# Performance work log

Hardware: AMD Instinct MI355X
Metric: run time of the kernel (lower is better)

## Reference

```python
import jax, jax.numpy as jnp
import numpy as np

B, IN_SEQ, HID_SEQ, OUT_SEQ = 2, 2048, 2048, 2048
C_IN, C_OUT, H = 1024, 1024, 16
HD = C_OUT // H  # 64


def _linear_params(key, out_f, in_f):
    kw, kb = jax.random.split(key)
    bound = 1.0 / np.sqrt(in_f)
    w = jax.random.uniform(kw, (out_f, in_f), jnp.float32, -bound, bound)
    b = jax.random.uniform(kb, (out_f,), jnp.float32, -bound, bound)
    return w, b


def setup_inputs() -> dict:
    key = jax.random.key(0)
    ks = jax.random.split(key, 6)
    x = jax.random.normal(ks[0], (B, IN_SEQ, C_IN), jnp.float32)
    w_hseq, b_hseq = _linear_params(ks[1], HID_SEQ, IN_SEQ)
    wq, bq = _linear_params(ks[2], C_OUT, C_IN)
    wk, bk = _linear_params(ks[3], C_OUT, C_IN)
    wv, bv = _linear_params(ks[4], C_OUT, C_IN)
    w_oseq, b_oseq = _linear_params(ks[5], OUT_SEQ, HID_SEQ)
    return {"x": x, "w_hseq": w_hseq, "b_hseq": b_hseq,
            "wq": wq, "bq": bq, "wk": wk, "bk": bk, "wv": wv, "bv": bv,
            "w_oseq": w_oseq, "b_oseq": b_oseq}


def reference(x, w_hseq, b_hseq, wq, bq, wk, bk, wv, bv, w_oseq, b_oseq):
    b = x.shape[0]
    # seq-axis projection: Linear(in_seq -> hidden_seq) applied to x.transpose(1,2)
    # xh[b, t, c] = sum_s x[b, s, c] * w_hseq[t, s] + b_hseq[t]
    xh = jnp.einsum('bsc,ts->btc', x, w_hseq) + b_hseq[:, None]
    q = (xh @ wq.T + bq).reshape(b, HID_SEQ, H, HD).transpose(0, 2, 1, 3)  # [B,H,Sh,hd]
    k = (xh @ wk.T + bk).reshape(b, HID_SEQ, H, HD).transpose(0, 2, 1, 3)
    v = (xh @ wv.T + bv).reshape(b, HID_SEQ, H, HD).transpose(0, 2, 1, 3)
    scores = jnp.einsum('bhqd,bhkd->bhqk', q, k) / np.sqrt(HD).astype(np.float32)
    attn = jax.nn.softmax(scores, axis=-1)                       # [B,H,Sh,Sh]
    flex = jnp.einsum('bhqk,ok->bhqo', attn, w_oseq) + b_oseq    # [B,H,Sh,So]
    # flexscale.transpose(-2,-1) @ v contracts over the QUERY axis q
    out = jnp.einsum('bhqo,bhqd->bhod', flex, v)                 # [B,H,So,hd]
    return out.transpose(0, 2, 1, 3).reshape(b, OUT_SEQ, C_OUT)
```

## Files before the change

kernel.cpp:

```cpp
#include <hip/hip_runtime.h>
#include <hip/hip_bf16.h>

typedef unsigned short u16;
typedef unsigned int u32;
typedef unsigned long long u64;
typedef __attribute__((ext_vector_type(8))) short s16x8;
typedef __attribute__((ext_vector_type(4))) float f32x4;
typedef __attribute__((ext_vector_type(16))) float f32x16;

#define SCL 0.1803368867f

#if __has_builtin(__builtin_amdgcn_exp2f)
#define EXP2(x) __builtin_amdgcn_exp2f(x)
#else
#define EXP2(x) exp2f(x)
#endif

__device__ __forceinline__ float bf2f(u16 v){ u32 u = ((u32)v)<<16; return __builtin_bit_cast(float,u); }
__device__ __forceinline__ u16 f2bf(float f){
  u32 u = __builtin_bit_cast(u32,f);
  u += 0x7fff + ((u>>16)&1);
  return (u16)(u>>16);
}
__device__ __forceinline__ u32 pkbf(float a, float b){
  u32 ua = __builtin_bit_cast(u32,a) + 0x8000u;
  u32 ub = __builtin_bit_cast(u32,b) + 0x8000u;
  return (ua>>16) | (ub & 0xFFFF0000u);
}
__device__ __forceinline__ void glds16(const u16* g, const u16* lds_u){
  __builtin_amdgcn_global_load_lds(
      (const __attribute__((address_space(1))) void*)(u64)g,
      (__attribute__((address_space(3))) void*)(u32)(u64)lds_u,
      16, 0, 0);
}
__device__ __forceinline__ f32x4 mfma16(s16x8 a, s16x8 b, f32x4 c){
  return __builtin_amdgcn_mfma_f32_16x16x32_bf16(a,b,c,0,0,0);
}
__device__ __forceinline__ f32x16 mfma32(s16x8 a, s16x8 b, f32x16 c){
  return __builtin_amdgcn_mfma_f32_32x32x16_bf16(a,b,c,0,0,0);
}

__global__ __launch_bounds__(256) void detect_dtype(const u16* __restrict__ x, u32* __restrict__ flag){
  __shared__ int cnt;
  if (threadIdx.x==0) cnt = 0;
  __syncthreads();
  int local = 0;
  for (int i = threadIdx.x; i < 4096; i += 256){
    u16 v = x[2*i];
    int e = (v>>7)&0xFF;
    if (e >= 140 || e <= 100) local++;
  }
  atomicAdd(&cnt, local);
  __syncthreads();
  if (threadIdx.x==0) *flag = (cnt > 1024) ? 1u : 0u;
}

struct CvtArgs { const void* src[10]; u16* dst[10]; int n[10]; };

__global__ __launch_bounds__(256) void convert_inputs(CvtArgs a, const u32* __restrict__ flag){
  const int which = blockIdx.y;
  const int n = a.n[which];
  const int base = blockIdx.x*2048 + threadIdx.x;
  if (base >= n) return;
  u16* dst = a.dst[which];
  if (*flag){
    const float* s = (const float*)a.src[which];
    #pragma unroll
    for (int j=0;j<8;j++){ int i = base + j*256; if (i<n) dst[i] = f2bf(s[i]); }
  } else {
    const u16* s = (const u16*)a.src[which];
    #pragma unroll
    for (int j=0;j<8;j++){ int i = base + j*256; if (i<n) dst[i] = s[i]; }
  }
}

__global__ __launch_bounds__(256) void transpose_x(
    const void* __restrict__ src, const u32* __restrict__ flag, u16* __restrict__ dst)
{
  __shared__ u16 T[64][72];
  const int s0 = blockIdx.x*64, c0 = blockIdx.y*64, b = blockIdx.z;
  const int t = threadIdx.x;
  const int r = t>>2, cc = (t&3)*16;
  const long off = ((long)(b*2048 + s0 + r))*1024 + c0 + cc;
  if (*flag){
    const float* p = (const float*)src + off;
    #pragma unroll
    for (int j=0;j<16;j++) T[r][cc+j] = f2bf(p[j]);
  } else {
    const u16* p = (const u16*)src + off;
    *(s16x8*)&T[r][cc]   = *(const s16x8*)p;
    *(s16x8*)&T[r][cc+8] = *(const s16x8*)(p+8);
  }
  __syncthreads();
  {
    const int orow = t&63, oc = (t>>6)*16;
    u16 tmp[16];
    #pragma unroll
    for (int j=0;j<16;j++) tmp[j] = T[oc+j][orow];
    u16* q = dst + (long)b*2097152 + (long)(c0+orow)*2048 + s0 + oc;
    *(s16x8*)q     = *(s16x8*)&tmp[0];
    *(s16x8*)(q+8) = *(s16x8*)&tmp[8];
  }
}

__global__ __launch_bounds__(256) void rowsum_part(const u16* __restrict__ qkv, float* __restrict__ svp){
  const int c = blockIdx.x*256 + threadIdx.x;
  const int b = c>>10, cc = c&1023;
  const int tz = blockIdx.y;
  const u16* p = qkv + ((long)(b*2048 + tz*256))*3072 + 2048 + cc;
  float s = 0.f;
  #pragma unroll 8
  for (int i=0;i<256;i++) s += bf2f(p[(long)i*3072]);
  svp[tz*2048 + c] = s;
}
__global__ __launch_bounds__(256) void rowsum_fin(const float* __restrict__ svp, float* __restrict__ sv){
  const int c = blockIdx.x*256 + threadIdx.x;
  float s = 0.f;
  #pragma unroll
  for (int z=0;z<8;z++) s += svp[z*2048 + c];
  sv[c] = s;
}

template<int BN, int BMODE, bool DYN, bool QS>
__global__ __launch_bounds__(256) void gemm_t(
    const u16* __restrict__ A, const u16* __restrict__ B,
    const u16* __restrict__ bias, const float* __restrict__ r1col,
    const u32* __restrict__ dflag, void* __restrict__ C,
    int K, int lda, int ldb, int ldc,
    long aBatch, long bBatch, long cBatch)
{
  constexpr int BM = 128;
  constexpr int ACH = BM/64, BCH = BN/64;
  constexpr int MI = (BN==128) ? 4 : 2;
  __shared__ u16 As[2][BM*32];
  __shared__ u16 Bs[2][BN*32];
  const int t = threadIdx.x, w = t>>6, quad = (t&63)>>4, l16 = t&15;
  const int z = blockIdx.z;
  const int m0 = blockIdx.x*BM, n0 = blockIdx.y*BN;
  const u16* Ag = A + (long)z*aBatch + (long)m0*lda;
  const u16* Bg = B + (long)z*bBatch + (long)n0*ldb;
  const int wm = (BN==128) ? (w>>1)*64 : w*32;
  const int wn = (BN==128) ? (w&1)*64 : 0;

  auto stage = [&](int buf, int k0){
    #pragma unroll
    for (int i=0;i<ACH;i++){
      const int chunk = i*256 + t;
      glds16(Ag + (long)(chunk>>2)*lda + k0 + (chunk&3)*8, &As[buf][(i*256 + w*64)*8]);
    }
    #pragma unroll
    for (int i=0;i<BCH;i++){
      const int chunk = i*256 + t;
      glds16(Bg + (long)(chunk>>2)*ldb + k0 + (chunk&3)*8, &Bs[buf][(i*256 + w*64)*8]);
    }
  };

  f32x4 acc[MI][4];
  #pragma unroll
  for (int i=0;i<MI;i++)
    #pragma unroll
    for (int j=0;j<4;j++) acc[i][j] = (f32x4){0.f,0.f,0.f,0.f};

  stage(0, 0);
  const int nk = K>>5;
  for (int kt=0; kt<nk; ++kt){
    __syncthreads();
    if (kt+1 < nk) stage((kt+1)&1, (kt+1)<<5);
    const u16* as = As[kt&1];
    const u16* bs = Bs[kt&1];
    s16x8 a[MI], bb[4];
    #pragma unroll
    for (int i=0;i<MI;i++) a[i] = *(const s16x8*)&as[(wm + i*16 + l16)*32 + quad*8];
    #pragma unroll
    for (int j=0;j<4;j++)  bb[j]= *(const s16x8*)&bs[(wn + j*16 + l16)*32 + quad*8];
    #pragma unroll
    for (int i=0;i<MI;i++)
      #pragma unroll
      for (int j=0;j<4;j++)
        acc[i][j] = mfma16(a[i], bb[j], acc[i][j]);
  }

  bool f32o = false;
  if (DYN) f32o = (*dflag != 0);
  #pragma unroll
  for (int i=0;i<MI;i++){
    #pragma unroll
    for (int j=0;j<4;j++){
      const int col = n0 + wn + j*16 + l16;
      #pragma unroll
      for (int r=0;r<4;r++){
        const int row = m0 + wm + i*16 + quad*4 + r;
        float vv = acc[i][j][r];
        if (BMODE==1) vv += bf2f(bias[row]);
        if (BMODE==2) vv += bf2f(bias[col]);
        if (BMODE==3) vv += bf2f(bias[row]) * r1col[z*1024 + col];
        if (QS){ if (col < 1024) vv *= SCL; }
        const long idx = (long)z*cBatch + (long)row*ldc + col;
        if (DYN && f32o) ((float*)C)[idx] = vv;
        else             ((u16*)C)[idx]   = f2bf(vv);
      }
    }
  }
}

__global__ __launch_bounds__(256) void attn_stats(const u16* __restrict__ qkv, u16* __restrict__ VtG){
  __shared__ u16 Qs[64][68];
  __shared__ u16 Ks[64][68];
  __shared__ float red[2][64];
  __shared__ float ilv[64];
  const int q0 = blockIdx.x*64, bh = blockIdx.y, b = bh>>4, h = bh&15;
  const int t = threadIdx.x, w = t>>6, l32 = t&31, half = (t&63)>>5;
  const int wq = w>>1, wk = w&1;
  {
    const int r = t>>2, cc = (t&3)*16;
    const u16* p = &qkv[((long)(b*2048 + q0 + r))*3072 + h*64 + cc];
    *(s16x8*)&Qs[r][cc]   = *(const s16x8*)p;
    *(s16x8*)&Qs[r][cc+8] = *(const s16x8*)(p+8);
  }
  __syncthreads();
  s16x8 aq[4];
  #pragma unroll
  for (int u=0;u<4;u++) aq[u] = *(s16x8*)&Qs[wq*32 + l32][u*16 + half*8];
  float lp[16];
  #pragma unroll
  for (int r=0;r<16;r++) lp[r] = 0.f;

  for (int kc=0; kc<2048; kc+=64){
    __syncthreads();
    {
      const int r = t>>2, cc = (t&3)*16;
      const u16* p = &qkv[((long)(b*2048 + kc + r))*3072 + 1024 + h*64 + cc];
      *(s16x8*)&Ks[r][cc]   = *(const s16x8*)p;
      *(s16x8*)&Ks[r][cc+8] = *(const s16x8*)(p+8);
    }
    __syncthreads();
    s16x8 kb[4];
    #pragma unroll
    for (int u=0;u<4;u++) kb[u] = *(s16x8*)&Ks[wk*32 + l32][u*16 + half*8];
    f32x16 acc = {};
    #pragma unroll
    for (int u=0;u<4;u++) acc = mfma32(aq[u], kb[u], acc);
    #pragma unroll
    for (int r=0;r<16;r++) lp[r] += EXP2(acc[r]);
  }
  #pragma unroll
  for (int off=1; off<32; off<<=1)
    #pragma unroll
    for (int r=0;r<16;r++) lp[r] += __shfl_xor(lp[r], off);
  if (l32 == 0){
    #pragma unroll
    for (int r=0;r<16;r++)
      red[wk][wq*32 + 4*half + (r&3) + 8*(r>>2)] = lp[r];
  }
  __syncthreads();
  if (t < 64) ilv[t] = 1.f / (red[0][t] + red[1][t]);
  __syncthreads();
  {
    const int r = t>>2, cc = (t&3)*16;
    const u16* p = &qkv[((long)(b*2048 + q0 + r))*3072 + 2048 + h*64 + cc];
    const float sc = ilv[r];
    s16x8 v0 = *(const s16x8*)p, v1 = *(const s16x8*)(p+8);
    #pragma unroll
    for (int j=0;j<8;j++){
      Qs[r][cc+j]   = f2bf(bf2f((u16)v0[j])*sc);
      Qs[r][cc+8+j] = f2bf(bf2f((u16)v1[j])*sc);
    }
  }
  __syncthreads();
  {
    const int orow = t&63, oc = (t>>6)*16;
    u16 tmp[16];
    #pragma unroll
    for (int j=0;j<16;j++) tmp[j] = Qs[oc+j][orow];
    u16* q = VtG + (long)b*2097152 + (long)(h*64+orow)*2048 + q0 + oc;
    *(s16x8*)q     = *(s16x8*)&tmp[0];
    *(s16x8*)(q+8) = *(s16x8*)&tmp[8];
  }
}

__global__ __launch_bounds__(256) void attn_pv(
    const u16* __restrict__ qkv, const u16* __restrict__ VtG, u16* __restrict__ Mt)
{
  __shared__ u16 KPs[64][68];
  __shared__ u16 Qs[64][68];
  __shared__ u16 Vs[64][68];
  const int k0 = blockIdx.x*64, bh = blockIdx.y, b = bh>>4, h = bh&15;
  const int t = threadIdx.x, w = t>>6, l32 = t&31, half = (t&63)>>5;
  const int wr = w>>1, wk = w&1;
  const int sr = t>>2, scc = (t&3)*16;
  {
    const u16* p = &qkv[((long)(b*2048 + k0 + sr))*3072 + 1024 + h*64 + scc];
    *(s16x8*)&KPs[sr][scc]   = *(const s16x8*)p;
    *(s16x8*)&KPs[sr][scc+8] = *(const s16x8*)(p+8);
  }
  __syncthreads();
  s16x8 kb[4];
  #pragma unroll
  for (int u=0;u<4;u++) kb[u] = *(s16x8*)&KPs[wk*32 + l32][u*16 + half*8];

  f32x16 accM = {};
  for (int q0=0; q0<2048; q0+=64){
    __syncthreads();
    {
      const u16* pq = &qkv[((long)(b*2048 + q0 + sr))*3072 + h*64 + scc];
      *(s16x8*)&Qs[sr][scc]   = *(const s16x8*)pq;
      *(s16x8*)&Qs[sr][scc+8] = *(const s16x8*)(pq+8);
      const u16* pv = &VtG[((long)(b*1024 + h*64 + sr))*2048 + q0 + scc];
      *(s16x8*)&Vs[sr][scc]   = *(const s16x8*)pv;
      *(s16x8*)&Vs[sr][scc+8] = *(const s16x8*)(pv+8);
    }
    __syncthreads();
    s16x8 aq[4];
    #pragma unroll
    for (int u=0;u<4;u++) aq[u] = *(s16x8*)&Qs[wr*32 + l32][u*16 + half*8];
    f32x16 acc = {};
    #pragma unroll
    for (int u=0;u<4;u++) acc = mfma32(aq[u], kb[u], acc);
    const int kcol = wk*32 + l32;
    #pragma unroll
    for (int g=0; g<4; g++){
      float p0 = EXP2(acc[4*g+0]);
      float p1 = EXP2(acc[4*g+1]);
      float p2 = EXP2(acc[4*g+2]);
      float p3 = EXP2(acc[4*g+3]);
      u64 v = (u64)pkbf(p0,p1) | ((u64)pkbf(p2,p3) << 32);
      *(u64*)&KPs[kcol][wr*32 + 8*g + 4*half] = v;
    }
    __syncthreads();
    s16x8 av[4], bp[4];
    #pragma unroll
    for (int u=0;u<4;u++) av[u] = *(s16x8*)&Vs[wr*32 + l32][u*16 + half*8];
    #pragma unroll
    for (int u=0;u<4;u++) bp[u] = *(s16x8*)&KPs[wk*32 + l32][u*16 + half*8];
    #pragma unroll
    for (int u=0;u<4;u++) accM = mfma32(av[u], bp[u], accM);
  }
  #pragma unroll
  for (int r=0;r<16;r++){
    const int d = wr*32 + 4*half + (r&3) + 8*(r>>2);
    const int k = k0 + wk*32 + l32;
    Mt[((long)(b*1024 + h*64 + d))*2048 + k] = f2bf(accM[r]);
  }
}

extern "C" void kernel_launch(void* const* d_in, const int* in_sizes, int n_in,
                              void* d_out, int out_size, void* d_ws, size_t ws_size,
                              hipStream_t stream)
{
  (void)n_in; (void)out_size; (void)ws_size;
  char* ws = (char*)d_ws;
  u32*  dflag = (u32*)ws;            ws += 64;
  u16*  whc   = (u16*)ws;            ws += (size_t)8388608;
  u16*  wqkvc = (u16*)ws;            ws += (size_t)6291456;
  u16*  woc   = (u16*)ws;            ws += (size_t)8388608;
  u16*  bhc   = (u16*)ws;            ws += 4096;
  u16*  bqkvc = (u16*)ws;            ws += 8192;
  u16*  boc   = (u16*)ws;            ws += 4096;
  u16*  xT    = (u16*)ws;            ws += (size_t)8388608;
  u16*  xh    = (u16*)ws;            ws += (size_t)8388608;
  u16*  qkvb  = (u16*)ws;            ws += (size_t)25165824;
  u16*  VtG   = (u16*)ws;            ws += (size_t)8388608;
  u16*  Mt    = (u16*)ws;            ws += (size_t)8388608;
  float* svp  = (float*)ws;          ws += (size_t)65536;
  float* sv   = (float*)ws;          ws += 8192;

  detect_dtype<<<1,256,0,stream>>>((const u16*)d_in[0], dflag);
  CvtArgs ca;
  const void* srcs[10] = {d_in[1], d_in[2], d_in[3], d_in[4], d_in[5],
                          d_in[6], d_in[7], d_in[8], d_in[9], d_in[10]};
  u16* dsts[10] = {whc, bhc, wqkvc, bqkvc, wqkvc+1048576, bqkvc+1024,
                   wqkvc+2097152, bqkvc+2048, woc, boc};
  const int ns[10] = {in_sizes[1], in_sizes[2], in_sizes[3], in_sizes[4], in_sizes[5],
                      in_sizes[6], in_sizes[7], in_sizes[8], in_sizes[9], in_sizes[10]};
  for (int i=0;i<10;i++){ ca.src[i]=srcs[i]; ca.dst[i]=dsts[i]; ca.n[i]=ns[i]; }
  convert_inputs<<<dim3(2048,10),256,0,stream>>>(ca, dflag);

  const long S2M = 2097152L;

  transpose_x<<<dim3(32,16,2),256,0,stream>>>(d_in[0], dflag, xT);

  gemm_t<64,1,false,false><<<dim3(16,16,2),256,0,stream>>>(whc, xT, bhc, nullptr, dflag, xh,
      2048, 2048, 2048, 1024, 0L, S2M, S2M);

  gemm_t<128,2,false,true><<<dim3(16,24,2),256,0,stream>>>(xh, wqkvc, bqkvc, nullptr, dflag, qkvb,
      1024, 1024, 1024, 3072, S2M, 0L, (long)2048*3072);

  rowsum_part<<<dim3(8,8),256,0,stream>>>(qkvb, svp);
  rowsum_fin<<<8,256,0,stream>>>(svp, sv);

  attn_stats<<<dim3(32,32),256,0,stream>>>(qkvb, VtG);

  attn_pv<<<dim3(32,32),256,0,stream>>>(qkvb, VtG, Mt);

  gemm_t<64,3,true,false><<<dim3(16,16,2),256,0,stream>>>(woc, Mt, boc, sv, dflag, d_out,
      2048, 2048, 2048, 1024, 0L, S2M, S2M);
}
```

Measured before the change: 362.4 us.

## Load Q/V/K fragments directly into registers with next-tile prefetch in attn_pv

```diff
diff --git a/kernel.cpp b/kernel.cpp
--- a/kernel.cpp
+++ b/kernel.cpp
@@ -281,59 +281,62 @@
 __global__ __launch_bounds__(256) void attn_pv(
     const u16* __restrict__ qkv, const u16* __restrict__ VtG, u16* __restrict__ Mt)
 {
-  __shared__ u16 KPs[64][68];
-  __shared__ u16 Qs[64][68];
-  __shared__ u16 Vs[64][68];
+  __shared__ u16 Ps[64][68];
+  __shared__ u16 pad[14336];
   const int k0 = blockIdx.x*64, bh = blockIdx.y, b = bh>>4, h = bh&15;
   const int t = threadIdx.x, w = t>>6, l32 = t&31, half = (t&63)>>5;
   const int wr = w>>1, wk = w&1;
-  const int sr = t>>2, scc = (t&3)*16;
-  {
-    const u16* p = &qkv[((long)(b*2048 + k0 + sr))*3072 + 1024 + h*64 + scc];
-    *(s16x8*)&KPs[sr][scc]   = *(const s16x8*)p;
-    *(s16x8*)&KPs[sr][scc+8] = *(const s16x8*)(p+8);
-  }
-  __syncthreads();
+  if (Mt == nullptr) ((volatile u16*)pad)[t] = 0;
+
+  const u16* kbase = qkv + ((long)(b*2048 + k0 + wk*32 + l32))*3072 + 1024 + h*64 + half*8;
   s16x8 kb[4];
   #pragma unroll
-  for (int u=0;u<4;u++) kb[u] = *(s16x8*)&KPs[wk*32 + l32][u*16 + half*8];
+  for (int u=0;u<4;u++) kb[u] = *(const s16x8*)(kbase + u*16);
+
+  const u16* qbase = qkv + ((long)(b*2048 + wr*32 + l32))*3072 + h*64 + half*8;
+  const u16* vbase = VtG + ((long)(b*1024 + h*64 + wr*32 + l32))*2048 + half*8;
+
+  s16x8 aq[4], av[4];
+  #pragma unroll
+  for (int u=0;u<4;u++) aq[u] = *(const s16x8*)(qbase + u*16);
+  #pragma unroll
+  for (int u=0;u<4;u++) av[u] = *(const s16x8*)(vbase + u*16);
 
   f32x16 accM = {};
-  for (int q0=0; q0<2048; q0+=64){
-    __syncthreads();
-    {
-      const u16* pq = &qkv[((long)(b*2048 + q0 + sr))*3072 + h*64 + scc];
-      *(s16x8*)&Qs[sr][scc]   = *(const s16x8*)pq;
-      *(s16x8*)&Qs[sr][scc+8] = *(const s16x8*)(pq+8);
-      const u16* pv = &VtG[((long)(b*1024 + h*64 + sr))*2048 + q0 + scc];
-      *(s16x8*)&Vs[sr][scc]   = *(const s16x8*)pv;
-      *(s16x8*)&Vs[sr][scc+8] = *(const s16x8*)(pv+8);
-    }
-    __syncthreads();
-    s16x8 aq[4];
-    #pragma unroll
-    for (int u=0;u<4;u++) aq[u] = *(s16x8*)&Qs[wr*32 + l32][u*16 + half*8];
+  const int kcol = wk*32 + l32;
+  for (int i=0; i<32; i++){
     f32x16 acc = {};
     #pragma unroll
     for (int u=0;u<4;u++) acc = mfma32(aq[u], kb[u], acc);
-    const int kcol = wk*32 + l32;
+    if (i < 31){
+      const u16* qn = qbase + (long)(i+1)*64*3072;
+      #pragma unroll
+      for (int u=0;u<4;u++) aq[u] = *(const s16x8*)(qn + u*16);
+    }
+    u64 pk[4];
     #pragma unroll
     for (int g=0; g<4; g++){
       float p0 = EXP2(acc[4*g+0]);
       float p1 = EXP2(acc[4*g+1]);
       float p2 = EXP2(acc[4*g+2]);
       float p3 = EXP2(acc[4*g+3]);
-      u64 v = (u64)pkbf(p0,p1) | ((u64)pkbf(p2,p3) << 32);
-      *(u64*)&KPs[kcol][wr*32 + 8*g + 4*half] = v;
+      pk[g] = (u64)pkbf(p0,p1) | ((u64)pkbf(p2,p3) << 32);
     }
     __syncthreads();
-    s16x8 av[4], bp[4];
-    #pragma unroll
-    for (int u=0;u<4;u++) av[u] = *(s16x8*)&Vs[wr*32 + l32][u*16 + half*8];
-    #pragma unroll
-    for (int u=0;u<4;u++) bp[u] = *(s16x8*)&KPs[wk*32 + l32][u*16 + half*8];
+    #pragma unroll
+    for (int g=0; g<4; g++)
+      *(u64*)&Ps[kcol][wr*32 + 8*g + 4*half] = pk[g];
+    __syncthreads();
+    s16x8 bp[4];
+    #pragma unroll
+    for (int u=0;u<4;u++) bp[u] = *(s16x8*)&Ps[wk*32 + l32][u*16 + half*8];
     #pragma unroll
     for (int u=0;u<4;u++) accM = mfma32(av[u], bp[u], accM);
+    if (i < 31){
+      const u16* vn = vbase + (i+1)*64;
+      #pragma unroll
+      for (int u=0;u<4;u++) av[u] = *(const s16x8*)(vn + u*16);
+    }
   }
   #pragma unroll
   for (int r=0;r<16;r++){
```

After: 405.9 us. 1.12x slower.
